# Kernel tuning notes

Hardware: AMD Instinct MI355X
Metric: run time of the kernel (lower is better)

The kernel has to match this reference:

```python
import jax, jax.numpy as jnp
import numpy as np

IN_FEATURES = 4096
OUT_FEATURES = 11008
BATCH = 16


def setup_inputs() -> dict:
    key = jax.random.key(0)
    k_x, k_w, k_s, k_b = jax.random.split(key, 4)
    x = jax.random.normal(k_x, (BATCH, IN_FEATURES), dtype=jnp.float32)
    # symmetric int8 weights stored as int32 for jax portability (values in [-127, 127])
    weight_int8 = jax.random.randint(k_w, (OUT_FEATURES, IN_FEATURES), -127, 128, dtype=jnp.int32)
    # per-output-channel scales, small positive values typical of int8 quantization
    weight_scale = jax.random.uniform(k_s, (OUT_FEATURES,), dtype=jnp.float32, minval=0.005, maxval=0.02)
    bias = jax.random.normal(k_b, (OUT_FEATURES,), dtype=jnp.float32)
    return {"x": x, "weight_int8": weight_int8, "weight_scale": weight_scale, "bias": bias}


def reference(x, weight_int8, weight_scale, bias):
    # Dequantize: w_dq[o, i] = int8[o, i] * scale[o]  -> fp32 [OUT, IN]
    w_dq = weight_int8.astype(x.dtype) * weight_scale[:, None]
    # F.linear: y = x @ w_dq.T + bias  -> [BATCH, OUT]
    return jnp.einsum("bi,oi->bo", x, w_dq) + bias
```

## Files before the change

kernel.cpp:

```cpp
#include <hip/hip_runtime.h>

#define IN_F   4096
#define OUT_F  11008
#define BATCH  16
#define CO     16
#define BLOCK  256
#define SPLITK 4
#define KCHUNK (IN_F / SPLITK)
#define NIT    (KCHUNK / 256)

typedef int   i32x4 __attribute__((ext_vector_type(4)));

__global__ __launch_bounds__(BLOCK) void init_out_kernel(
    const float* __restrict__ bias, float* __restrict__ out)
{
    int idx = blockIdx.x * BLOCK + threadIdx.x;
    if (idx < BATCH * OUT_F) {
        int o = idx % OUT_F;
        out[idx] = bias[o];
    }
}

__global__ __launch_bounds__(BLOCK) void qlin_kernel(
    const float* __restrict__ x,
    const int*   __restrict__ w,
    const float* __restrict__ scale,
    float* __restrict__ out)
{
    __shared__ float xs[BATCH][KCHUNK];

    const int tid = threadIdx.x;
    const int tx  = tid & 63;
    const int ty  = tid >> 6;
    const int o0  = blockIdx.x * CO + ty * 4;
    const int kb  = blockIdx.y * KCHUNK;

    const i32x4* __restrict__ wbase = (const i32x4*)(w + (size_t)o0 * IN_F);

    float acc[64];
    #pragma unroll
    for (int i = 0; i < 64; ++i) acc[i] = 0.f;

    #pragma unroll
    for (int j = 0; j < (BATCH * KCHUNK / 4) / BLOCK; ++j) {
        int f  = tid + j * BLOCK;
        int b  = f >> 8;
        int kc = f & 255;
        const float* src = x + (size_t)b * IN_F + kb + kc * 4;
        void* dst = (char*)&xs[0][0] + (size_t)f * 16;
        __builtin_amdgcn_global_load_lds(
            (const __attribute__((address_space(1))) void*)src,
            (__attribute__((address_space(3))) void*)dst,
            16, 0, 0);
    }
    __syncthreads();

    i32x4 wr[NIT][4];
    #pragma unroll
    for (int it = 0; it < NIT; ++it) {
        const size_t kg4 = (size_t)((kb >> 2) + it * 64 + tx);
        #pragma unroll
        for (int r = 0; r < 4; ++r)
            wr[it][r] = __builtin_nontemporal_load(wbase + kg4 + (size_t)r * (IN_F / 4));
    }

    #pragma unroll
    for (int it = 0; it < NIT; ++it) {
        const int kl = it * 256 + tx * 4;

        float wf[4][4];
        #pragma unroll
        for (int r = 0; r < 4; ++r)
            #pragma unroll
            for (int e = 0; e < 4; ++e)
                wf[r][e] = (float)wr[it][r][e];

        #pragma unroll
        for (int bc = 0; bc < 4; ++bc) {
            float4 xv[4];
            #pragma unroll
            for (int bb = 0; bb < 4; ++bb)
                xv[bb] = *(const float4*)&xs[bc * 4 + bb][kl];

            #pragma unroll
            for (int r = 0; r < 4; ++r)
                #pragma unroll
                for (int bb = 0; bb < 4; ++bb) {
                    float a = acc[r * 16 + bc * 4 + bb];
                    a += wf[r][0] * xv[bb].x;
                    a += wf[r][1] * xv[bb].y;
                    a += wf[r][2] * xv[bb].z;
                    a += wf[r][3] * xv[bb].w;
                    acc[r * 16 + bc * 4 + bb] = a;
                }
        }
    }

    #pragma unroll
    for (int wd = 32; wd >= 1; wd >>= 1) {
        const bool upper = (tx & wd) != 0;
        #pragma unroll
        for (int i = 0; i < wd; ++i) {
            float lo = acc[i]      + __shfl_xor(acc[i],      wd);
            float hi = acc[i + wd] + __shfl_xor(acc[i + wd], wd);
            acc[i] = upper ? hi : lo;
        }
    }

    const int o = o0 + (tx >> 4);
    const int b = tx & 15;
    atomicAdd(&out[(size_t)b * OUT_F + o], acc[0] * scale[o]);
}

extern "C" void kernel_launch(void* const* d_in, const int* in_sizes, int n_in,
                              void* d_out, int out_size, void* d_ws, size_t ws_size,
                              hipStream_t stream) {
    const float* x     = (const float*)d_in[0];
    const int*   w     = (const int*)d_in[1];
    const float* scale = (const float*)d_in[2];
    const float* bias  = (const float*)d_in[3];
    float* out = (float*)d_out;

    init_out_kernel<<<(BATCH * OUT_F + BLOCK - 1) / BLOCK, BLOCK, 0, stream>>>(bias, out);

    dim3 grid(OUT_F / CO, SPLITK);
    qlin_kernel<<<grid, dim3(BLOCK), 0, stream>>>(x, w, scale, out);
}
```

Before: 264.1 us.

## Remove split-K, loop over K with double-buffered LDS x stages

Replaces the split-K grid with atomics by a single block per 16 output channels that loops over the full K in 512-wide stages. The x tile for each stage is double-buffered in LDS so the next stage loads while the current one computes. Bias and scale are fused into a direct store, which removes the init kernel and the atomics. In exchange the grid shrinks to 688 blocks, and each block has fewer weight loads in flight per iteration, which lowers memory parallelism on a bandwidth-bound 180MB weight stream.

```diff
diff --git a/kernel.cpp b/kernel.cpp
--- a/kernel.cpp
+++ b/kernel.cpp
@@ -5,35 +5,24 @@
 #define BATCH  16
 #define CO     16
 #define BLOCK  256
-#define SPLITK 4
-#define KCHUNK (IN_F / SPLITK)
-#define NIT    (KCHUNK / 256)
+#define STAGE  512
+#define NST    (IN_F / STAGE)
 
 typedef int   i32x4 __attribute__((ext_vector_type(4)));
-
-__global__ __launch_bounds__(BLOCK) void init_out_kernel(
-    const float* __restrict__ bias, float* __restrict__ out)
-{
-    int idx = blockIdx.x * BLOCK + threadIdx.x;
-    if (idx < BATCH * OUT_F) {
-        int o = idx % OUT_F;
-        out[idx] = bias[o];
-    }
-}
 
 __global__ __launch_bounds__(BLOCK) void qlin_kernel(
     const float* __restrict__ x,
     const int*   __restrict__ w,
     const float* __restrict__ scale,
+    const float* __restrict__ bias,
     float* __restrict__ out)
 {
-    __shared__ float xs[BATCH][KCHUNK];
+    __shared__ float xs[2][BATCH][STAGE];
 
     const int tid = threadIdx.x;
     const int tx  = tid & 63;
     const int ty  = tid >> 6;
     const int o0  = blockIdx.x * CO + ty * 4;
-    const int kb  = blockIdx.y * KCHUNK;
 
     const i32x4* __restrict__ wbase = (const i32x4*)(w + (size_t)o0 * IN_F);
 
@@ -41,59 +30,70 @@
     #pragma unroll
     for (int i = 0; i < 64; ++i) acc[i] = 0.f;
 
-    #pragma unroll
-    for (int j = 0; j < (BATCH * KCHUNK / 4) / BLOCK; ++j) {
-        int f  = tid + j * BLOCK;
-        int b  = f >> 8;
-        int kc = f & 255;
-        const float* src = x + (size_t)b * IN_F + kb + kc * 4;
-        void* dst = (char*)&xs[0][0] + (size_t)f * 16;
-        __builtin_amdgcn_global_load_lds(
-            (const __attribute__((address_space(1))) void*)src,
-            (__attribute__((address_space(3))) void*)dst,
-            16, 0, 0);
-    }
+    auto stage_load = [&](int s, int buf) {
+        #pragma unroll
+        for (int j = 0; j < (BATCH * STAGE / 4) / BLOCK; ++j) {
+            int f  = tid + j * BLOCK;
+            int b  = f >> 7;
+            int kc = f & 127;
+            const float* src = x + (size_t)b * IN_F + s * STAGE + kc * 4;
+            void* dst = (char*)&xs[buf][0][0] + (size_t)f * 16;
+            __builtin_amdgcn_global_load_lds(
+                (const __attribute__((address_space(1))) void*)src,
+                (__attribute__((address_space(3))) void*)dst,
+                16, 0, 0);
+        }
+    };
+
+    stage_load(0, 0);
     __syncthreads();
 
-    i32x4 wr[NIT][4];
-    #pragma unroll
-    for (int it = 0; it < NIT; ++it) {
-        const size_t kg4 = (size_t)((kb >> 2) + it * 64 + tx);
+    for (int s = 0; s < NST; ++s) {
+        const int cur = s & 1;
+        if (s + 1 < NST) stage_load(s + 1, cur ^ 1);
+
+        i32x4 wr[2][4];
         #pragma unroll
-        for (int r = 0; r < 4; ++r)
-            wr[it][r] = __builtin_nontemporal_load(wbase + kg4 + (size_t)r * (IN_F / 4));
-    }
-
-    #pragma unroll
-    for (int it = 0; it < NIT; ++it) {
-        const int kl = it * 256 + tx * 4;
-
-        float wf[4][4];
-        #pragma unroll
-        for (int r = 0; r < 4; ++r)
+        for (int it = 0; it < 2; ++it) {
+            const size_t kg4 = (size_t)(s * 128 + it * 64 + tx);
             #pragma unroll
-            for (int e = 0; e < 4; ++e)
-                wf[r][e] = (float)wr[it][r][e];
+            for (int r = 0; r < 4; ++r)
+                wr[it][r] = __builtin_nontemporal_load(wbase + kg4 + (size_t)r * (IN_F / 4));
+        }
 
         #pragma unroll
-        for (int bc = 0; bc < 4; ++bc) {
-            float4 xv[4];
-            #pragma unroll
-            for (int bb = 0; bb < 4; ++bb)
-                xv[bb] = *(const float4*)&xs[bc * 4 + bb][kl];
+        for (int it = 0; it < 2; ++it) {
+            const int kl = it * 256 + tx * 4;
 
+            float wf[4][4];
             #pragma unroll
             for (int r = 0; r < 4; ++r)
                 #pragma unroll
-                for (int bb = 0; bb < 4; ++bb) {
-                    float a = acc[r * 16 + bc * 4 + bb];
-                    a += wf[r][0] * xv[bb].x;
-                    a += wf[r][1] * xv[bb].y;
-                    a += wf[r][2] * xv[bb].z;
-                    a += wf[r][3] * xv[bb].w;
-                    acc[r * 16 + bc * 4 + bb] = a;
-                }
+                for (int e = 0; e < 4; ++e)
+                    wf[r][e] = (float)wr[it][r][e];
+
+            #pragma unroll
+            for (int bc = 0; bc < 4; ++bc) {
+                float4 xv[4];
+                #pragma unroll
+                for (int bb = 0; bb < 4; ++bb)
+                    xv[bb] = *(const float4*)&xs[cur][bc * 4 + bb][kl];
+
+                #pragma unroll
+                for (int r = 0; r < 4; ++r)
+                    #pragma unroll
+                    for (int bb = 0; bb < 4; ++bb) {
+                        float a = acc[r * 16 + bc * 4 + bb];
+                        a += wf[r][0] * xv[bb].x;
+                        a += wf[r][1] * xv[bb].y;
+                        a += wf[r][2] * xv[bb].z;
+                        a += wf[r][3] * xv[bb].w;
+                        acc[r * 16 + bc * 4 + bb] = a;
+                    }
+            }
         }
+
+        __syncthreads();
     }
 
     #pragma unroll
@@ -109,7 +109,7 @@
 
     const int o = o0 + (tx >> 4);
     const int b = tx & 15;
-    atomicAdd(&out[(size_t)b * OUT_F + o], acc[0] * scale[o]);
+    out[(size_t)b * OUT_F + o] = fmaf(acc[0], scale[o], bias[o]);
 }
 
 extern "C" void kernel_launch(void* const* d_in, const int* in_sizes, int n_in,
@@ -121,8 +121,5 @@
     const float* bias  = (const float*)d_in[3];
     float* out = (float*)d_out;
 
-    init_out_kernel<<<(BATCH * OUT_F + BLOCK - 1) / BLOCK, BLOCK, 0, stream>>>(bias, out);
-
-    dim3 grid(OUT_F / CO, SPLITK);
-    qlin_kernel<<<grid, dim3(BLOCK), 0, stream>>>(x, w, scale, out);
+    qlin_kernel<<<dim3(OUT_F / CO), dim3(BLOCK), 0, stream>>>(x, w, scale, bias, out);
 }
```

Measured after the change: 265.6 us. About the same (+0.6%).

## Double-buffer x tiles in LDS per K stage and raise occupancy hint

Applied to the files above, without the earlier changes.

Replaces the single upfront load of the whole 16x1024 x chunk into LDS with a two-buffer ring of 256-wide stages, prefetching the next stage while computing on the current one. LDS per block drops from 64KB to 32KB and launch bounds request 3 blocks per SM, aiming for more concurrent blocks to hide weight-load latency. In exchange, weight loads are no longer all issued upfront (only 4 per stage), adding a barrier per stage and possibly exposing more memory latency per block.

```diff
diff --git a/kernel.cpp b/kernel.cpp
--- a/kernel.cpp
+++ b/kernel.cpp
@@ -7,7 +7,8 @@
 #define BLOCK  256
 #define SPLITK 4
 #define KCHUNK (IN_F / SPLITK)
-#define NIT    (KCHUNK / 256)
+#define STAGE  256
+#define NST    (KCHUNK / STAGE)
 
 typedef int   i32x4 __attribute__((ext_vector_type(4)));
 
@@ -21,13 +22,13 @@
     }
 }
 
-__global__ __launch_bounds__(BLOCK) void qlin_kernel(
+__global__ __launch_bounds__(BLOCK, 3) void qlin_kernel(
     const float* __restrict__ x,
     const int*   __restrict__ w,
     const float* __restrict__ scale,
     float* __restrict__ out)
 {
-    __shared__ float xs[BATCH][KCHUNK];
+    __shared__ float xs[2][BATCH][STAGE];
 
     const int tid = threadIdx.x;
     const int tx  = tid & 63;
@@ -41,46 +42,50 @@
     #pragma unroll
     for (int i = 0; i < 64; ++i) acc[i] = 0.f;
 
-    #pragma unroll
-    for (int j = 0; j < (BATCH * KCHUNK / 4) / BLOCK; ++j) {
-        int f  = tid + j * BLOCK;
-        int b  = f >> 8;
-        int kc = f & 255;
-        const float* src = x + (size_t)b * IN_F + kb + kc * 4;
-        void* dst = (char*)&xs[0][0] + (size_t)f * 16;
-        __builtin_amdgcn_global_load_lds(
-            (const __attribute__((address_space(1))) void*)src,
-            (__attribute__((address_space(3))) void*)dst,
-            16, 0, 0);
-    }
+    auto stage_load = [&](int s, int buf) {
+        #pragma unroll
+        for (int j = 0; j < (BATCH * STAGE / 4) / BLOCK; ++j) {
+            int f  = tid + j * BLOCK;
+            int b  = f >> 6;
+            int kc = f & 63;
+            const float* src = x + (size_t)b * IN_F + kb + s * STAGE + kc * 4;
+            void* dst = (char*)&xs[buf][0][0] + (size_t)f * 16;
+            __builtin_amdgcn_global_load_lds(
+                (const __attribute__((address_space(1))) void*)src,
+                (__attribute__((address_space(3))) void*)dst,
+                16, 0, 0);
+        }
+    };
+
+    stage_load(0, 0);
     __syncthreads();
 
-    i32x4 wr[NIT][4];
-    #pragma unroll
-    for (int it = 0; it < NIT; ++it) {
-        const size_t kg4 = (size_t)((kb >> 2) + it * 64 + tx);
+    for (int s = 0; s < NST; ++s) {
+        const int cur = s & 1;
+
+        const size_t kg4 = (size_t)((kb + s * STAGE) >> 2) + tx;
+        i32x4 wr[4];
         #pragma unroll
         for (int r = 0; r < 4; ++r)
-            wr[it][r] = __builtin_nontemporal_load(wbase + kg4 + (size_t)r * (IN_F / 4));
-    }
+            wr[r] = __builtin_nontemporal_load(wbase + kg4 + (size_t)r * (IN_F / 4));
 
-    #pragma unroll
-    for (int it = 0; it < NIT; ++it) {
-        const int kl = it * 256 + tx * 4;
+        if (s + 1 < NST) stage_load(s + 1, cur ^ 1);
 
         float wf[4][4];
         #pragma unroll
         for (int r = 0; r < 4; ++r)
             #pragma unroll
             for (int e = 0; e < 4; ++e)
-                wf[r][e] = (float)wr[it][r][e];
+                wf[r][e] = (float)wr[r][e];
+
+        const int kl = tx * 4;
 
         #pragma unroll
         for (int bc = 0; bc < 4; ++bc) {
             float4 xv[4];
             #pragma unroll
             for (int bb = 0; bb < 4; ++bb)
-                xv[bb] = *(const float4*)&xs[bc * 4 + bb][kl];
+                xv[bb] = *(const float4*)&xs[cur][bc * 4 + bb][kl];
 
             #pragma unroll
             for (int r = 0; r < 4; ++r)
@@ -94,6 +99,8 @@
                     acc[r * 16 + bc * 4 + bb] = a;
                 }
         }
+
+        __syncthreads();
     }
 
     #pragma unroll
```

Measured after the change: 260.9 us. No clear change (-1.2%).
